# Kernel tuning notes

Hardware: AMD Instinct MI355X
Metric: run time of the kernel (lower is better)

## Reference

```python
import jax, jax.numpy as jnp
import numpy as np

B, S, N, F, H, O = 4, 16, 1024, 64, 128, 64
L_LAYERS, N_HEADS, CHUNK = 3, 4, 128
EPS = 1e-5


def setup_inputs() -> dict:
    key = jax.random.key(0)
    ks = jax.random.split(key, 16)
    adj = (jax.random.uniform(ks[0], (B, S, N, N)) < 0.05).astype(jnp.float32)
    adj = adj * (1.0 - jnp.eye(N, dtype=jnp.float32))
    x = jax.random.normal(ks[1], (B, S, F), dtype=jnp.float32)
    mask = jnp.ones((B, S), dtype=jnp.float32)
    sd = lambda fan_in: 1.0 / np.sqrt(fan_in)
    inp = {
        "x": x, "adj": adj, "mask": mask,
        "feature_importance": jnp.ones((F,), jnp.float32),
        "W_in": jax.random.normal(ks[2], (F, H)) * sd(F),
        "b_in": jnp.zeros((H,), jnp.float32),
        "ln_g": jnp.ones((H,), jnp.float32),
        "ln_b": jnp.zeros((H,), jnp.float32),
        "gcn_W": jax.random.normal(ks[3], (L_LAYERS, H, H)) * sd(H),
        "gcn_b": jnp.zeros((L_LAYERS, H), jnp.float32),
        "bn_g": jnp.ones((L_LAYERS, H), jnp.float32),
        "bn_b": jnp.zeros((L_LAYERS, H), jnp.float32),
        "Wqkv": jax.random.normal(ks[4], (3 * H, H)) * sd(H),
        "bqkv": jnp.zeros((3 * H,), jnp.float32),
        "Wo": jax.random.normal(ks[5], (H, H)) * sd(H),
        "bo": jnp.zeros((H,), jnp.float32),
        "W_out": jax.random.normal(ks[6], (H, O)) * sd(H),
        "b_out": jnp.zeros((O,), jnp.float32),
    }
    return inp


def _chunked_mha(h, Wqkv, bqkv, Wo, bo):
    # h: [B,S,N,H]; attention within chunks of CHUNK nodes (torch MHA, eval mode)
    b, s, n, hdim = h.shape
    c, dh = n // CHUNK, hdim // N_HEADS
    xr = h.reshape(b, s, c, CHUNK, hdim)
    qkv = xr @ Wqkv.T + bqkv                      # [B,S,C,L,3H]
    q, k, v = jnp.split(qkv, 3, axis=-1)
    split = lambda t: t.reshape(b, s, c, CHUNK, N_HEADS, dh).swapaxes(-3, -2)  # [B,S,C,nh,L,dh]
    q, k, v = split(q) * (dh ** -0.5), split(k), split(v)
    attn = jax.nn.softmax(jnp.einsum('bscnld,bscnmd->bscnlm', q, k), axis=-1)
    o = jnp.einsum('bscnlm,bscnmd->bscnld', attn, v)
    o = o.swapaxes(-3, -2).reshape(b, s, c, CHUNK, hdim) @ Wo.T + bo
    return o.reshape(b, s, n, hdim)


def reference(x, adj, mask, feature_importance, W_in, b_in, ln_g, ln_b,
              gcn_W, gcn_b, bn_g, bn_b, Wqkv, bqkv, Wo, bo, W_out, b_out):
    b, s, f = x.shape
    n = adj.shape[-1]
    # feature scaling + input projection + layer norm (same vector for all nodes)
    xv = (x * feature_importance) @ W_in + b_in            # [B,S,H]
    mu = xv.mean(-1, keepdims=True)
    var = ((xv - mu) ** 2).mean(-1, keepdims=True)
    hv = (xv - mu) / jnp.sqrt(var + EPS) * ln_g + ln_b
    h = jnp.broadcast_to(hv[:, :, None, :], (b, s, n, hv.shape[-1]))  # [B,S,N,H]
    h_init = h
    # GCN normalization: D^{-1/2} (A + I) D^{-1/2}
    A_hat = adj + jnp.eye(n, dtype=adj.dtype)
    dinv = jax.lax.rsqrt(A_hat.sum(-1))                     # [B,S,N]
    A_norm = dinv[..., :, None] * A_hat * dinv[..., None, :]
    bn_scale = 1.0 / np.sqrt(1.0 + EPS)  # eval BN, running mean 0 / var 1
    for l in range(L_LAYERS):
        hw = h @ gcn_W[l]
        hc = jnp.einsum('bsnm,bsmh->bsnh', A_norm, hw) + gcn_b[l]
        hc = hc * bn_scale * bn_g[l] + bn_b[l]
        hc = _chunked_mha(hc, Wqkv, bqkv, Wo, bo)
        hc = jax.nn.relu(hc)  # dropout = identity in eval
        h = h + hc            # use_skip (num_layers > 1)
    h = h + h_init
    node_embeddings = h @ W_out + b_out                    # [B,S,N,O]
    graph_embeddings = node_embeddings.mean(axis=2)        # [B,S,O]
    graph_embeddings = graph_embeddings * mask[:, :, None]
    node_embeddings = node_embeddings * mask[:, :, None, None]
    return node_embeddings, graph_embeddings
```

## Files before the change

kernel.cpp:

```cpp
#include <hip/hip_runtime.h>

typedef __bf16 bf16_t;
typedef bf16_t bf16x8 __attribute__((ext_vector_type(8)));
typedef float f32x4 __attribute__((ext_vector_type(4)));

#define DEV static __device__ __forceinline__

constexpr float kBnScale = 0.999995000037499375f;

DEV unsigned short f2bf(float f) {
  unsigned u = __builtin_bit_cast(unsigned, f);
  u += 0x7fffu + ((u >> 16) & 1u);
  return (unsigned short)(u >> 16);
}
DEV float bf2f(unsigned short s) {
  return __builtin_bit_cast(float, ((unsigned)s) << 16);
}
DEV f32x4 mfma16(bf16x8 a, bf16x8 b, f32x4 c) {
  return __builtin_amdgcn_mfma_f32_16x16x32_bf16(a, b, c, 0, 0, 0);
}
DEV unsigned swz(unsigned byteoff, unsigned row) { return byteoff ^ ((row & 7u) << 4); }

__global__ __launch_bounds__(256) void k_pre(
    const float* __restrict__ adj, unsigned short* __restrict__ cols,
    int* __restrict__ cnt, float* __restrict__ dinv,
    const float* __restrict__ x, const float* __restrict__ fi,
    const float* __restrict__ Win, const float* __restrict__ bin,
    const float* __restrict__ lng, const float* __restrict__ lnb,
    const float* __restrict__ gW, const float* __restrict__ bng,
    float* __restrict__ hv, float* __restrict__ hw0s,
    const float* __restrict__ Wqkv, const float* __restrict__ Wo,
    const float* __restrict__ Wout,
    unsigned short* __restrict__ WqkvB, unsigned short* __restrict__ WoB,
    unsigned short* __restrict__ gWB, unsigned short* __restrict__ WoutB) {
  const int bid = blockIdx.x;
  if (bid < 16384) {
    const int w = threadIdx.x >> 6, lane = threadIdx.x & 63;
    const long row = (long)bid * 4 + w;
    const float* ap = adj + row * 1024;
    unsigned short* cp = cols + row * 128;
    int c = 0;
#pragma unroll
    for (int it = 0; it < 4; ++it) {
      const float4 v4 = *(const float4*)(ap + it * 256 + lane * 4);
      const float vv[4] = {v4.x, v4.y, v4.z, v4.w};
#pragma unroll
      for (int j = 0; j < 4; ++j) {
        const unsigned long long m = __ballot(vv[j] != 0.0f);
        const int pos = c + __popcll(m & ((1ull << lane) - 1ull));
        if (vv[j] != 0.0f && pos < 128) cp[pos] = (unsigned short)(it * 256 + lane * 4 + j);
        c += __popcll(m);
      }
    }
    if (lane == 0) {
      cnt[row] = c;
      dinv[row] = 1.0f / sqrtf((float)(c + 1));
    }
  } else if (bid < 16448) {
    __shared__ float sred[2], sred2[2], shv[128];
    const int bs = bid - 16384, t = threadIdx.x;
    float accv = 0.f, d = 0.f;
    if (t < 128) {
      accv = bin[t];
      for (int f = 0; f < 64; ++f) accv += x[bs * 64 + f] * fi[f] * Win[f * 128 + t];
      float ssum = accv;
      for (int m = 1; m < 64; m <<= 1) ssum += __shfl_xor(ssum, m);
      if ((t & 63) == 0) sred[t >> 6] = ssum;
    }
    __syncthreads();
    const float mu = (sred[0] + sred[1]) * (1.0f / 128.0f);
    if (t < 128) {
      d = accv - mu;
      float vs = d * d;
      for (int m = 1; m < 64; m <<= 1) vs += __shfl_xor(vs, m);
      if ((t & 63) == 0) sred2[t >> 6] = vs;
    }
    __syncthreads();
    const float var = (sred2[0] + sred2[1]) * (1.0f / 128.0f);
    if (t < 128) {
      const float h = d / sqrtf(var + 1e-5f) * lng[t] + lnb[t];
      hv[bs * 128 + t] = h;
      shv[t] = h;
    }
    __syncthreads();
    if (t < 128) {
      float a2 = 0.f;
      for (int k = 0; k < 128; ++k) a2 += shv[k] * gW[k * 128 + t];
      hw0s[bs * 128 + t] = a2 * kBnScale * bng[t];
    }
  } else {
    const int i = (bid - 16448) * 256 + threadIdx.x;
    if (i < 49152) {
      WqkvB[i] = f2bf(Wqkv[i]);
    } else if (i < 65536) {
      const int j = i - 49152;
      WoB[j] = f2bf(Wo[j]);
    } else if (i < 114688) {
      const int j = i - 65536, l = j >> 14, r = j & 16383, n = r >> 7, k = r & 127;
      gWB[j] = f2bf(gW[(l << 14) + k * 128 + n]);
    } else {
      const int j = i - 114688, n = j >> 7, k = j & 127;
      WoutB[j] = f2bf(Wout[k * 64 + n]);
    }
  }
}

__global__ __launch_bounds__(256) void k_scal(const unsigned short* __restrict__ cols,
                                              const int* __restrict__ cnt, const float* __restrict__ dinv,
                                              float* __restrict__ S) {
  const int w = threadIdx.x >> 6, lane = threadIdx.x & 63;
  const long row = (long)blockIdx.x * 4 + w;
  const int cn = cnt[row] < 128 ? cnt[row] : 128;
  const long bsbase = row & ~1023L;
  const int c0 = cols[row * 128 + lane];
  const int c1 = cols[row * 128 + 64 + lane];
  float s = 0.f;
  if (lane < cn) s += dinv[bsbase + c0];
  if (lane + 64 < cn) s += dinv[bsbase + c1];
  for (int m = 1; m < 64; m <<= 1) s += __shfl_xor(s, m);
  if (lane == 0) {
    const float d = dinv[row];
    S[row] = d * (d + s);
  }
}

template <bool L0>
__global__ __launch_bounds__(256) void k_qkv(const unsigned short* __restrict__ hc,
                                             const unsigned short* __restrict__ WqkvB,
                                             const float* __restrict__ bqkv,
                                             const float* __restrict__ S, const float* __restrict__ hw0s,
                                             const float* __restrict__ gb0, const float* __restrict__ bng0,
                                             const float* __restrict__ bnb0,
                                             unsigned short* __restrict__ qkvb) {
  __shared__ __align__(16) unsigned short Ab[128 * 128];
  __shared__ __align__(16) unsigned short Bb[128 * 128];
  const int t = threadIdx.x;
  const long blockRow = (long)blockIdx.x * 128;
  const int pan = blockIdx.y;
  const int bs = (int)(blockRow >> 10);

  if constexpr (L0) {
#pragma unroll
    for (int i = 0; i < 16; ++i) {
      const int f = (t + i * 256) * 4;
      const unsigned row = f >> 7, k = f & 127;
      const float Sr = S[blockRow + row];
      const float4 hw = *(const float4*)(hw0s + bs * 128 + k);
      const float4 gv = *(const float4*)(gb0 + k);
      const float4 bg = *(const float4*)(bng0 + k);
      const float4 bb = *(const float4*)(bnb0 + k);
      float4 v;
      v.x = Sr * hw.x + (gv.x * kBnScale * bg.x + bb.x);
      v.y = Sr * hw.y + (gv.y * kBnScale * bg.y + bb.y);
      v.z = Sr * hw.z + (gv.z * kBnScale * bg.z + bb.z);
      v.w = Sr * hw.w + (gv.w * kBnScale * bg.w + bb.w);
      uint2 u;
      u.x = f2bf(v.x) | ((unsigned)f2bf(v.y) << 16);
      u.y = f2bf(v.z) | ((unsigned)f2bf(v.w) << 16);
      *(uint2*)(Ab + (swz(row * 256u + k * 2u, row) >> 1)) = u;
    }
  } else {
#pragma unroll
    for (int i = 0; i < 8; ++i) {
      const int f = (t + i * 256) * 8;
      const unsigned row = f >> 7, k = f & 127;
      *(uint4*)(Ab + (swz(row * 256u + k * 2u, row) >> 1)) = *(const uint4*)(hc + blockRow * 128 + f);
    }
  }
#pragma unroll
  for (int i = 0; i < 8; ++i) {
    const int f = (t + i * 256) * 8;
    const unsigned n = f >> 7, k = f & 127;
    *(uint4*)(Bb + (swz(n * 256u + k * 2u, n) >> 1)) = *(const uint4*)(WqkvB + pan * 16384 + f);
  }
  __syncthreads();

  const int lane = t & 63, w = t >> 6, wr = w >> 1, wc = w & 1;
  const f32x4 vzero = {0.f, 0.f, 0.f, 0.f};
  f32x4 acc[4][4];
#pragma unroll
  for (int a = 0; a < 4; ++a)
#pragma unroll
    for (int b = 0; b < 4; ++b) acc[a][b] = vzero;
#pragma unroll
  for (int kk = 0; kk < 4; ++kk) {
    const unsigned kb = kk * 64u + (unsigned)((lane >> 4) << 4);
    bf16x8 af[4], bfr[4];
#pragma unroll
    for (int mt = 0; mt < 4; ++mt) {
      const unsigned row = wr * 64 + mt * 16 + (lane & 15);
      af[mt] = *(const bf16x8*)(Ab + (swz(row * 256u + kb, row) >> 1));
    }
#pragma unroll
    for (int nt = 0; nt < 4; ++nt) {
      const unsigned col = wc * 64 + nt * 16 + (lane & 15);
      bfr[nt] = *(const bf16x8*)(Bb + (swz(col * 256u + kb, col) >> 1));
    }
#pragma unroll
    for (int mt = 0; mt < 4; ++mt)
#pragma unroll
      for (int nt = 0; nt < 4; ++nt) acc[mt][nt] = mfma16(af[mt], bfr[nt], acc[mt][nt]);
  }
#pragma unroll
  for (int mt = 0; mt < 4; ++mt)
#pragma unroll
    for (int nt = 0; nt < 4; ++nt)
#pragma unroll
      for (int r = 0; r < 4; ++r) {
        const long gRow = blockRow + wr * 64 + mt * 16 + ((lane >> 4) << 2) + r;
        const int gCol = wc * 64 + nt * 16 + (lane & 15);
        qkvb[gRow * 384 + pan * 128 + gCol] = f2bf(acc[mt][nt][r] + bqkv[pan * 128 + gCol]);
      }
}

__global__ __launch_bounds__(256) void k_spmm(const unsigned* __restrict__ hwp,
                                              const unsigned short* __restrict__ cols,
                                              const int* __restrict__ cnt, const float* __restrict__ dinv,
                                              const float* __restrict__ gb, const float* __restrict__ bng,
                                              const float* __restrict__ bnb, unsigned* __restrict__ hc) {
  int b = blockIdx.x;
  b = (b & 7) * 2048 + (b >> 3);
  const int w = threadIdx.x >> 6, lane = threadIdx.x & 63;
  const long row = (long)b * 4 + w;
  __shared__ unsigned short scol[4][128];
  scol[w][lane] = cols[row * 128 + lane];
  scol[w][lane + 64] = cols[row * 128 + 64 + lane];
  const int cn = cnt[row] < 128 ? cnt[row] : 128;
  const long bsbase = row & ~1023L;
  const unsigned us = hwp[row * 64 + lane];
  float a0 = bf2f((unsigned short)us), a1 = bf2f((unsigned short)(us >> 16));
  int i = 0;
  for (; i + 4 <= cn; i += 4) {
    const uint2 jj = *(const uint2*)(&scol[w][i]);
    const int j0 = jj.x & 0xffff, j1 = jj.x >> 16, j2 = jj.y & 0xffff, j3 = jj.y >> 16;
    const unsigned u0 = hwp[(bsbase + j0) * 64 + lane];
    const unsigned u1 = hwp[(bsbase + j1) * 64 + lane];
    const unsigned u2 = hwp[(bsbase + j2) * 64 + lane];
    const unsigned u3 = hwp[(bsbase + j3) * 64 + lane];
    a0 += bf2f((unsigned short)u0) + bf2f((unsigned short)u1) + bf2f((unsigned short)u2) + bf2f((unsigned short)u3);
    a1 += bf2f((unsigned short)(u0 >> 16)) + bf2f((unsigned short)(u1 >> 16)) +
          bf2f((unsigned short)(u2 >> 16)) + bf2f((unsigned short)(u3 >> 16));
  }
  for (; i < cn; ++i) {
    const unsigned uu = hwp[(bsbase + scol[w][i]) * 64 + lane];
    a0 += bf2f((unsigned short)uu);
    a1 += bf2f((unsigned short)(uu >> 16));
  }
  const float di = dinv[row];
  const int c0 = lane * 2, c1 = c0 + 1;
  const float o0 = (di * a0 + gb[c0]) * (kBnScale * bng[c0]) + bnb[c0];
  const float o1 = (di * a1 + gb[c1]) * (kBnScale * bng[c1]) + bnb[c1];
  hc[row * 64 + lane] = (unsigned)f2bf(o0) | ((unsigned)f2bf(o1) << 16);
}

template <int MODE>
__global__ __launch_bounds__(256, 2) void k_af(
    const unsigned short* __restrict__ qkv,
    const unsigned short* __restrict__ WoB, const unsigned short* __restrict__ B2,
    const float* __restrict__ bo, const float* __restrict__ hv,
    const float* __restrict__ dinv, const float* __restrict__ bout,
    const float* __restrict__ mask,
    float* __restrict__ hbuf, unsigned short* __restrict__ hwp,
    float* __restrict__ ne, float* __restrict__ gpart) {
  __shared__ __align__(16) unsigned short sm[32768];
  unsigned short* Ab = sm;
  unsigned short* Bb = sm + 16384;
  const int t = threadIdx.x, lane = t & 63, hd = t >> 6;
  const int g = lane >> 4, l15 = lane & 15;
  const long cb = (long)blockIdx.x * 128;
  const int bs = (int)(cb >> 10);
  const f32x4 vzero = {0.f, 0.f, 0.f, 0.f};

  {
    const int m = t >> 1, half = t & 1;
    const unsigned short* vrow = qkv + (cb + m) * 384 + 256 + half * 64;
#pragma unroll
    for (int c8 = 0; c8 < 8; ++c8) {
      const uint4 u = *(const uint4*)(vrow + c8 * 8);
      const int col0 = half * 64 + c8 * 8;
      unsigned short* vb = Ab + (col0 >> 5) * 4096;
      const int dh0 = col0 & 31;
      const unsigned short e[8] = {(unsigned short)u.x, (unsigned short)(u.x >> 16),
                                   (unsigned short)u.y, (unsigned short)(u.y >> 16),
                                   (unsigned short)u.z, (unsigned short)(u.z >> 16),
                                   (unsigned short)u.w, (unsigned short)(u.w >> 16)};
#pragma unroll
      for (int j = 0; j < 8; ++j) {
        const unsigned dh = dh0 + j;
        vb[swz(dh * 256u + (unsigned)m * 2u, dh) >> 1] = e[j];
      }
    }
  }
  bf16x8 kf[8];
#pragma unroll
  for (int nt = 0; nt < 8; ++nt)
    kf[nt] = *(const bf16x8*)(qkv + (cb + nt * 16 + l15) * 384 + 128 + hd * 32 + (g << 3));
  __syncthreads();

  const unsigned short* vbb = Ab + hd * 4096;
  unsigned short* pb = Bb + hd * 4096;
  const float SC = 0.17677669529663687f * 1.4426950408889634f;
  unsigned pk[4][2][2][2];

#pragma unroll 1
  for (int p = 0; p < 4; ++p) {
    bf16x8 qf[2];
#pragma unroll
    for (int mt = 0; mt < 2; ++mt)
      qf[mt] = *(const bf16x8*)(qkv + (cb + p * 32 + mt * 16 + l15) * 384 + hd * 32 + (g << 3));
    f32x4 s[2][8];
#pragma unroll
    for (int mt = 0; mt < 2; ++mt)
#pragma unroll
      for (int nt = 0; nt < 8; ++nt) s[mt][nt] = vzero;
#pragma unroll
    for (int nt = 0; nt < 8; ++nt)
#pragma unroll
      for (int mt = 0; mt < 2; ++mt) s[mt][nt] = mfma16(qf[mt], kf[nt], s[mt][nt]);

    float rinv[2][4];
#pragma unroll
    for (int mt = 0; mt < 2; ++mt) {
#pragma unroll
      for (int r = 0; r < 4; ++r) {
        float mx = s[mt][0][r];
#pragma unroll
        for (int nt = 1; nt < 8; ++nt) mx = fmaxf(mx, s[mt][nt][r]);
#pragma unroll
        for (int msk = 1; msk < 16; msk <<= 1) mx = fmaxf(mx, __shfl_xor(mx, msk));
        const unsigned qp = mt * 16 + g * 4 + r;
        float sum = 0.f;
#pragma unroll
        for (int nt = 0; nt < 8; ++nt) {
          const float e = exp2f((s[mt][nt][r] - mx) * SC);
          sum += e;
          pb[swz(qp * 256u + (nt * 16 + l15) * 2u, qp) >> 1] = f2bf(e);
        }
#pragma unroll
        for (int msk = 1; msk < 16; msk <<= 1) sum += __shfl_xor(sum, msk);
        rinv[mt][r] = 1.0f / sum;
      }
    }

    f32x4 o[2][2];
#pragma unroll
    for (int mt = 0; mt < 2; ++mt)
#pragma unroll
      for (int nt = 0; nt < 2; ++nt) o[mt][nt] = vzero;
#pragma unroll
    for (int kk = 0; kk < 4; ++kk) {
      const unsigned kb = kk * 64u + (unsigned)(g << 4);
      bf16x8 pa[2], vf[2];
#pragma unroll
      for (int mt = 0; mt < 2; ++mt) {
        const unsigned rq = mt * 16 + l15;
        pa[mt] = *(const bf16x8*)(pb + (swz(rq * 256u + kb, rq) >> 1));
      }
#pragma unroll
      for (int nt = 0; nt < 2; ++nt) {
        const unsigned dh = nt * 16 + l15;
        vf[nt] = *(const bf16x8*)(vbb + (swz(dh * 256u + kb, dh) >> 1));
      }
#pragma unroll
      for (int mt = 0; mt < 2; ++mt)
#pragma unroll
        for (int nt = 0; nt < 2; ++nt) o[mt][nt] = mfma16(pa[mt], vf[nt], o[mt][nt]);
    }
#pragma unroll
    for (int mt = 0; mt < 2; ++mt)
#pragma unroll
      for (int nt = 0; nt < 2; ++nt) {
        pk[p][mt][nt][0] = (unsigned)f2bf(o[mt][nt][0] * rinv[mt][0]) |
                           ((unsigned)f2bf(o[mt][nt][1] * rinv[mt][1]) << 16);
        pk[p][mt][nt][1] = (unsigned)f2bf(o[mt][nt][2] * rinv[mt][2]) |
                           ((unsigned)f2bf(o[mt][nt][3] * rinv[mt][3]) << 16);
      }
  }
  __syncthreads();

#pragma unroll
  for (int p = 0; p < 4; ++p)
#pragma unroll
    for (int mt = 0; mt < 2; ++mt)
#pragma unroll
      for (int nt = 0; nt < 2; ++nt)
#pragma unroll
        for (int rr = 0; rr < 2; ++rr) {
          const unsigned u = pk[p][mt][nt][rr];
          const unsigned row0 = p * 32 + mt * 16 + g * 4 + rr * 2;
          const unsigned col = hd * 32 + nt * 16 + l15;
          Ab[swz(row0 * 256u + col * 2u, row0) >> 1] = (unsigned short)u;
          Ab[swz((row0 + 1) * 256u + col * 2u, row0 + 1) >> 1] = (unsigned short)(u >> 16);
        }
#pragma unroll
  for (int i = 0; i < 8; ++i) {
    const int f = (t + i * 256) * 8;
    const unsigned n = f >> 7, k = f & 127;
    *(uint4*)(Bb + (swz(n * 256u + k * 2u, n) >> 1)) = *(const uint4*)(WoB + f);
  }
  __syncthreads();

  const int wr = hd >> 1, wc = hd & 1;
  f32x4 acc[4][4];
#pragma unroll
  for (int a = 0; a < 4; ++a)
#pragma unroll
    for (int b = 0; b < 4; ++b) acc[a][b] = vzero;
#pragma unroll
  for (int kk = 0; kk < 4; ++kk) {
    const unsigned kb = kk * 64u + (unsigned)(g << 4);
    bf16x8 af[4], bfr[4];
#pragma unroll
    for (int mt = 0; mt < 4; ++mt) {
      const unsigned row = wr * 64 + mt * 16 + l15;
      af[mt] = *(const bf16x8*)(Ab + (swz(row * 256u + kb, row) >> 1));
    }
#pragma unroll
    for (int nt = 0; nt < 4; ++nt) {
      const unsigned col = wc * 64 + nt * 16 + l15;
      bfr[nt] = *(const bf16x8*)(Bb + (swz(col * 256u + kb, col) >> 1));
    }
#pragma unroll
    for (int mt = 0; mt < 4; ++mt)
#pragma unroll
      for (int nt = 0; nt < 4; ++nt) acc[mt][nt] = mfma16(af[mt], bfr[nt], acc[mt][nt]);
  }
  __syncthreads();

  {
    const float b0 = bo[wc * 64 + l15], b1 = bo[wc * 64 + 16 + l15];
    const float b2c = bo[wc * 64 + 32 + l15], b3c = bo[wc * 64 + 48 + l15];
    const float bb[4] = {b0, b1, b2c, b3c};
    float hb[4];
#pragma unroll
    for (int nt = 0; nt < 4; ++nt) hb[nt] = hv[bs * 128 + wc * 64 + nt * 16 + l15];
#pragma unroll
    for (int mt = 0; mt < 4; ++mt)
#pragma unroll
      for (int nt = 0; nt < 4; ++nt)
#pragma unroll
        for (int r = 0; r < 4; ++r) {
          const unsigned row = wr * 64 + mt * 16 + g * 4 + r;
          const long gRow = cb + row;
          const unsigned col = wc * 64 + nt * 16 + l15;
          float v = acc[mt][nt][r] + bb[nt];
          v = v > 0.f ? v : 0.f;
          if constexpr (MODE == 0) {
            v += hb[nt];
          } else {
            v += hbuf[gRow * 128 + col];
            if constexpr (MODE == 2) v += hb[nt];
          }
          if constexpr (MODE < 2) hbuf[gRow * 128 + col] = v;
          Ab[swz(row * 256u + col * 2u, row) >> 1] = f2bf(v);
        }
  }
  if constexpr (MODE < 2) {
#pragma unroll
    for (int i = 0; i < 8; ++i) {
      const int f = (t + i * 256) * 8;
      const unsigned n = f >> 7, k = f & 127;
      *(uint4*)(Bb + (swz(n * 256u + k * 2u, n) >> 1)) = *(const uint4*)(B2 + f);
    }
  } else {
#pragma unroll
    for (int i = 0; i < 4; ++i) {
      const int f = (t + i * 256) * 8;
      const unsigned n = f >> 7, k = f & 127;
      *(uint4*)(Bb + (swz(n * 256u + k * 2u, n) >> 1)) = *(const uint4*)(B2 + f);
    }
  }
  __syncthreads();

  if constexpr (MODE < 2) {
#pragma unroll
    for (int a = 0; a < 4; ++a)
#pragma unroll
      for (int b = 0; b < 4; ++b) acc[a][b] = vzero;
#pragma unroll
    for (int kk = 0; kk < 4; ++kk) {
      const unsigned kb = kk * 64u + (unsigned)(g << 4);
      bf16x8 af[4], bfr[4];
#pragma unroll
      for (int mt = 0; mt < 4; ++mt) {
        const unsigned row = wr * 64 + mt * 16 + l15;
        af[mt] = *(const bf16x8*)(Ab + (swz(row * 256u + kb, row) >> 1));
      }
#pragma unroll
      for (int nt = 0; nt < 4; ++nt) {
        const unsigned col = wc * 64 + nt * 16 + l15;
        bfr[nt] = *(const bf16x8*)(Bb + (swz(col * 256u + kb, col) >> 1));
      }
#pragma unroll
      for (int mt = 0; mt < 4; ++mt)
#pragma unroll
        for (int nt = 0; nt < 4; ++nt) acc[mt][nt] = mfma16(af[mt], bfr[nt], acc[mt][nt]);
    }
#pragma unroll
    for (int mt = 0; mt < 4; ++mt)
#pragma unroll
      for (int nt = 0; nt < 4; ++nt)
#pragma unroll
        for (int r = 0; r < 4; ++r) {
          const long gRow = cb + wr * 64 + mt * 16 + g * 4 + r;
          const unsigned col = wc * 64 + nt * 16 + l15;
          hwp[gRow * 128 + col] = f2bf(acc[mt][nt][r] * dinv[gRow]);
        }
  } else {
    f32x4 acc2[4][2];
#pragma unroll
    for (int a = 0; a < 4; ++a)
#pragma unroll
      for (int b = 0; b < 2; ++b) acc2[a][b] = vzero;
#pragma unroll
    for (int kk = 0; kk < 4; ++kk) {
      const unsigned kb = kk * 64u + (unsigned)(g << 4);
      bf16x8 af[4], bfr[2];
#pragma unroll
      for (int mt = 0; mt < 4; ++mt) {
        const unsigned row = wr * 64 + mt * 16 + l15;
        af[mt] = *(const bf16x8*)(Ab + (swz(row * 256u + kb, row) >> 1));
      }
#pragma unroll
      for (int nt = 0; nt < 2; ++nt) {
        const unsigned col = wc * 32 + nt * 16 + l15;
        bfr[nt] = *(const bf16x8*)(Bb + (swz(col * 256u + kb, col) >> 1));
      }
#pragma unroll
      for (int mt = 0; mt < 4; ++mt)
#pragma unroll
        for (int nt = 0; nt < 2; ++nt) acc2[mt][nt] = mfma16(af[mt], bfr[nt], acc2[mt][nt]);
    }
    const float mk = mask[bs];
#pragma unroll
    for (int nt = 0; nt < 2; ++nt) {
      const unsigned col = wc * 32 + nt * 16 + l15;
      const float b2 = bout[col];
      float csum = 0.f;
#pragma unroll
      for (int mt = 0; mt < 4; ++mt)
#pragma unroll
        for (int r = 0; r < 4; ++r) {
          const long gRow = cb + wr * 64 + mt * 16 + g * 4 + r;
          const float v = (acc2[mt][nt][r] + b2) * mk;
          ne[gRow * 64 + col] = v;
          csum += v;
        }
      csum += __shfl_xor(csum, 16);
      csum += __shfl_xor(csum, 32);
      if (g == 0) gpart[((long)blockIdx.x * 2 + wr) * 64 + col] = csum;
    }
  }
}

__global__ void k_gfin(const float* __restrict__ gpart, float* __restrict__ ge) {
  const int tid = blockIdx.x * 256 + threadIdx.x;
  if (tid >= 4096) return;
  const int bs = tid >> 6, col = tid & 63;
  float s = 0.f;
#pragma unroll
  for (int q = 0; q < 16; ++q) s += gpart[(bs * 16 + q) * 64 + col];
  ge[tid] = s * (1.0f / 1024.0f);
}

extern "C" void kernel_launch(void* const* d_in, const int* in_sizes, int n_in,
                              void* d_out, int out_size, void* d_ws, size_t ws_size,
                              hipStream_t stream) {
  const float* x = (const float*)d_in[0];
  const float* adj = (const float*)d_in[1];
  const float* mask = (const float*)d_in[2];
  const float* fi = (const float*)d_in[3];
  const float* Win = (const float*)d_in[4];
  const float* bin = (const float*)d_in[5];
  const float* lng = (const float*)d_in[6];
  const float* lnb = (const float*)d_in[7];
  const float* gW = (const float*)d_in[8];
  const float* gB = (const float*)d_in[9];
  const float* bng = (const float*)d_in[10];
  const float* bnb = (const float*)d_in[11];
  const float* Wqkv = (const float*)d_in[12];
  const float* bqkv = (const float*)d_in[13];
  const float* Wo = (const float*)d_in[14];
  const float* bo = (const float*)d_in[15];
  const float* Wout = (const float*)d_in[16];
  const float* bout = (const float*)d_in[17];

  char* ws = (char*)d_ws;
  float* dinv = (float*)ws;                    ws += 65536 * 4;
  int* cnt = (int*)ws;                         ws += 65536 * 4;
  float* S = (float*)ws;                       ws += 65536 * 4;
  float* hv = (float*)ws;                      ws += 64 * 128 * 4;
  float* hw0s = (float*)ws;                    ws += 64 * 128 * 4;
  float* gpart = (float*)ws;                   ws += 1024 * 64 * 4;
  unsigned short* WqkvB = (unsigned short*)ws; ws += 49152 * 2;
  unsigned short* WoB = (unsigned short*)ws;   ws += 16384 * 2;
  unsigned short* gWB = (unsigned short*)ws;   ws += 49152 * 2;
  unsigned short* WoutB = (unsigned short*)ws; ws += 8192 * 2;
  unsigned short* cols = (unsigned short*)ws;  ws += (size_t)65536 * 128 * 2;
  float* hbuf = (float*)ws;                    ws += (size_t)65536 * 128 * 4;
  unsigned short* hwp = (unsigned short*)ws;   ws += (size_t)65536 * 128 * 2;
  unsigned short* hc = (unsigned short*)ws;    ws += (size_t)65536 * 128 * 2;
  unsigned short* qkvb = (unsigned short*)ws;  ws += (size_t)65536 * 384 * 2;

  float* ne = (float*)d_out;
  float* ge = ne + (size_t)4194304;

  k_pre<<<16928, 256, 0, stream>>>(adj, cols, cnt, dinv, x, fi, Win, bin, lng, lnb,
                                   gW, bng, hv, hw0s, Wqkv, Wo, Wout,
                                   WqkvB, WoB, gWB, WoutB);
  k_scal<<<16384, 256, 0, stream>>>(cols, cnt, dinv, S);

  k_qkv<true><<<dim3(512, 3), 256, 0, stream>>>(nullptr, WqkvB, bqkv, S, hw0s, gB, bng, bnb, qkvb);
  k_af<0><<<512, 256, 0, stream>>>(qkvb, WoB, gWB + 16384, bo, hv, dinv, nullptr, nullptr,
                                   hbuf, hwp, nullptr, nullptr);
  k_spmm<<<16384, 256, 0, stream>>>((const unsigned*)hwp, cols, cnt, dinv,
                                    gB + 128, bng + 128, bnb + 128, (unsigned*)hc);
  k_qkv<false><<<dim3(512, 3), 256, 0, stream>>>(hc, WqkvB, bqkv, nullptr, nullptr, nullptr, nullptr, nullptr, qkvb);
  k_af<1><<<512, 256, 0, stream>>>(qkvb, WoB, gWB + 32768, bo, hv, dinv, nullptr, nullptr,
                                   hbuf, hwp, nullptr, nullptr);
  k_spmm<<<16384, 256, 0, stream>>>((const unsigned*)hwp, cols, cnt, dinv,
                                    gB + 256, bng + 256, bnb + 256, (unsigned*)hc);
  k_qkv<false><<<dim3(512, 3), 256, 0, stream>>>(hc, WqkvB, bqkv, nullptr, nullptr, nullptr, nullptr, nullptr, qkvb);
  k_af<2><<<512, 256, 0, stream>>>(qkvb, WoB, WoutB, bo, hv, dinv, bout, mask,
                                   hbuf, nullptr, ne, gpart);

  k_gfin<<<16, 256, 0, stream>>>(gpart, ge);
}
```

Measured before the change: 362.6 us.

## Vectorize SpMM gathers, remap blocks across XCDs, fuse layer-0 input into scaling kernel

The SpMM gather now has each 16-lane group fetch a whole 256-byte row as uint4 loads, with four neighbours handled in parallel and the partial sums combined by cross-lane shuffles. Before, each lane did a 4-byte load per neighbour. The scaling kernel now writes the layer-0 bf16 GCN output directly, so the QKV GEMM no longer needs a special first-layer path or the S buffer. Block indices in several kernels are permuted so that consecutive work lands on the same XCD, which should improve L2 locality. The costs are extra shuffle reductions and one more global write and read of the layer-0 activations.

```diff
diff --git a/kernel.cpp b/kernel.cpp
--- a/kernel.cpp
+++ b/kernel.cpp
@@ -35,8 +35,9 @@
     unsigned short* __restrict__ gWB, unsigned short* __restrict__ WoutB) {
   const int bid = blockIdx.x;
   if (bid < 16384) {
+    const int c4 = (bid & 7) * 2048 + (bid >> 3);
     const int w = threadIdx.x >> 6, lane = threadIdx.x & 63;
-    const long row = (long)bid * 4 + w;
+    const long row = (long)c4 * 4 + w;
     const float* ap = adj + row * 1024;
     unsigned short* cp = cols + row * 128;
     int c = 0;
@@ -105,11 +106,16 @@
   }
 }
 
-__global__ __launch_bounds__(256) void k_scal(const unsigned short* __restrict__ cols,
-                                              const int* __restrict__ cnt, const float* __restrict__ dinv,
-                                              float* __restrict__ S) {
+__global__ __launch_bounds__(256) void k_scal2(const unsigned short* __restrict__ cols,
+                                               const int* __restrict__ cnt, const float* __restrict__ dinv,
+                                               const float* __restrict__ hw0s,
+                                               const float* __restrict__ gb0, const float* __restrict__ bng0,
+                                               const float* __restrict__ bnb0,
+                                               unsigned* __restrict__ hc0) {
+  int b = blockIdx.x;
+  b = (b & 7) * 2048 + (b >> 3);
   const int w = threadIdx.x >> 6, lane = threadIdx.x & 63;
-  const long row = (long)blockIdx.x * 4 + w;
+  const long row = (long)b * 4 + w;
   const int cn = cnt[row] < 128 ? cnt[row] : 128;
   const long bsbase = row & ~1023L;
   const int c0 = cols[row * 128 + lane];
@@ -118,59 +124,35 @@
   if (lane < cn) s += dinv[bsbase + c0];
   if (lane + 64 < cn) s += dinv[bsbase + c1];
   for (int m = 1; m < 64; m <<= 1) s += __shfl_xor(s, m);
-  if (lane == 0) {
-    const float d = dinv[row];
-    S[row] = d * (d + s);
-  }
-}
-
-template <bool L0>
+  const float d = dinv[row];
+  const float S = d * (d + s);
+  const int bs = (int)(row >> 10);
+  const float2 hw = ((const float2*)hw0s)[bs * 64 + lane];
+  const float2 g2 = ((const float2*)gb0)[lane];
+  const float2 bg = ((const float2*)bng0)[lane];
+  const float2 bb = ((const float2*)bnb0)[lane];
+  const float v0 = S * hw.x + (g2.x * kBnScale * bg.x + bb.x);
+  const float v1 = S * hw.y + (g2.y * kBnScale * bg.y + bb.y);
+  hc0[row * 64 + lane] = (unsigned)f2bf(v0) | ((unsigned)f2bf(v1) << 16);
+}
+
 __global__ __launch_bounds__(256) void k_qkv(const unsigned short* __restrict__ hc,
                                              const unsigned short* __restrict__ WqkvB,
                                              const float* __restrict__ bqkv,
-                                             const float* __restrict__ S, const float* __restrict__ hw0s,
-                                             const float* __restrict__ gb0, const float* __restrict__ bng0,
-                                             const float* __restrict__ bnb0,
                                              unsigned short* __restrict__ qkvb) {
   __shared__ __align__(16) unsigned short Ab[128 * 128];
   __shared__ __align__(16) unsigned short Bb[128 * 128];
   const int t = threadIdx.x;
-  const long blockRow = (long)blockIdx.x * 128;
+  const int cx = (blockIdx.x & 7) * 64 + (blockIdx.x >> 3);
+  const long blockRow = (long)cx * 128;
   const int pan = blockIdx.y;
-  const int bs = (int)(blockRow >> 10);
-
-  if constexpr (L0) {
-#pragma unroll
-    for (int i = 0; i < 16; ++i) {
-      const int f = (t + i * 256) * 4;
-      const unsigned row = f >> 7, k = f & 127;
-      const float Sr = S[blockRow + row];
-      const float4 hw = *(const float4*)(hw0s + bs * 128 + k);
-      const float4 gv = *(const float4*)(gb0 + k);
-      const float4 bg = *(const float4*)(bng0 + k);
-      const float4 bb = *(const float4*)(bnb0 + k);
-      float4 v;
-      v.x = Sr * hw.x + (gv.x * kBnScale * bg.x + bb.x);
-      v.y = Sr * hw.y + (gv.y * kBnScale * bg.y + bb.y);
-      v.z = Sr * hw.z + (gv.z * kBnScale * bg.z + bb.z);
-      v.w = Sr * hw.w + (gv.w * kBnScale * bg.w + bb.w);
-      uint2 u;
-      u.x = f2bf(v.x) | ((unsigned)f2bf(v.y) << 16);
-      u.y = f2bf(v.z) | ((unsigned)f2bf(v.w) << 16);
-      *(uint2*)(Ab + (swz(row * 256u + k * 2u, row) >> 1)) = u;
-    }
-  } else {
-#pragma unroll
-    for (int i = 0; i < 8; ++i) {
-      const int f = (t + i * 256) * 8;
-      const unsigned row = f >> 7, k = f & 127;
-      *(uint4*)(Ab + (swz(row * 256u + k * 2u, row) >> 1)) = *(const uint4*)(hc + blockRow * 128 + f);
-    }
-  }
+
 #pragma unroll
   for (int i = 0; i < 8; ++i) {
     const int f = (t + i * 256) * 8;
-    const unsigned n = f >> 7, k = f & 127;
+    const unsigned row = f >> 7, k = f & 127;
+    *(uint4*)(Ab + (swz(row * 256u + k * 2u, row) >> 1)) = *(const uint4*)(hc + blockRow * 128 + f);
+    const unsigned n = row;
     *(uint4*)(Bb + (swz(n * 256u + k * 2u, n) >> 1)) = *(const uint4*)(WqkvB + pan * 16384 + f);
   }
   __syncthreads();
@@ -213,44 +195,81 @@
       }
 }
 
-__global__ __launch_bounds__(256) void k_spmm(const unsigned* __restrict__ hwp,
+__global__ __launch_bounds__(256) void k_spmm(const uint4* __restrict__ hwp16,
                                               const unsigned short* __restrict__ cols,
                                               const int* __restrict__ cnt, const float* __restrict__ dinv,
                                               const float* __restrict__ gb, const float* __restrict__ bng,
-                                              const float* __restrict__ bnb, unsigned* __restrict__ hc) {
+                                              const float* __restrict__ bnb, uint4* __restrict__ hc16) {
   int b = blockIdx.x;
   b = (b & 7) * 2048 + (b >> 3);
   const int w = threadIdx.x >> 6, lane = threadIdx.x & 63;
+  const int g = lane >> 4, l15 = lane & 15;
   const long row = (long)b * 4 + w;
   __shared__ unsigned short scol[4][128];
   scol[w][lane] = cols[row * 128 + lane];
   scol[w][lane + 64] = cols[row * 128 + 64 + lane];
   const int cn = cnt[row] < 128 ? cnt[row] : 128;
   const long bsbase = row & ~1023L;
-  const unsigned us = hwp[row * 64 + lane];
-  float a0 = bf2f((unsigned short)us), a1 = bf2f((unsigned short)(us >> 16));
-  int i = 0;
-  for (; i + 4 <= cn; i += 4) {
-    const uint2 jj = *(const uint2*)(&scol[w][i]);
-    const int j0 = jj.x & 0xffff, j1 = jj.x >> 16, j2 = jj.y & 0xffff, j3 = jj.y >> 16;
-    const unsigned u0 = hwp[(bsbase + j0) * 64 + lane];
-    const unsigned u1 = hwp[(bsbase + j1) * 64 + lane];
-    const unsigned u2 = hwp[(bsbase + j2) * 64 + lane];
-    const unsigned u3 = hwp[(bsbase + j3) * 64 + lane];
-    a0 += bf2f((unsigned short)u0) + bf2f((unsigned short)u1) + bf2f((unsigned short)u2) + bf2f((unsigned short)u3);
-    a1 += bf2f((unsigned short)(u0 >> 16)) + bf2f((unsigned short)(u1 >> 16)) +
-          bf2f((unsigned short)(u2 >> 16)) + bf2f((unsigned short)(u3 >> 16));
-  }
-  for (; i < cn; ++i) {
-    const unsigned uu = hwp[(bsbase + scol[w][i]) * 64 + lane];
-    a0 += bf2f((unsigned short)uu);
-    a1 += bf2f((unsigned short)(uu >> 16));
-  }
-  const float di = dinv[row];
-  const int c0 = lane * 2, c1 = c0 + 1;
-  const float o0 = (di * a0 + gb[c0]) * (kBnScale * bng[c0]) + bnb[c0];
-  const float o1 = (di * a1 + gb[c1]) * (kBnScale * bng[c1]) + bnb[c1];
-  hc[row * 64 + lane] = (unsigned)f2bf(o0) | ((unsigned)f2bf(o1) << 16);
+  float acc[8];
+#pragma unroll
+  for (int e = 0; e < 8; ++e) acc[e] = 0.f;
+  if (g == 0) {
+    const uint4 u = hwp16[row * 16 + l15];
+    const unsigned uu[4] = {u.x, u.y, u.z, u.w};
+#pragma unroll
+    for (int e2 = 0; e2 < 4; ++e2) {
+      acc[e2 * 2] += bf2f((unsigned short)uu[e2]);
+      acc[e2 * 2 + 1] += bf2f((unsigned short)(uu[e2] >> 16));
+    }
+  }
+  const int cn4 = cn & ~3;
+#pragma unroll 2
+  for (int i = 0; i < cn4; i += 4) {
+    const int j = scol[w][i + g];
+    const uint4 u = hwp16[(bsbase + j) * 16 + l15];
+    const unsigned uu[4] = {u.x, u.y, u.z, u.w};
+#pragma unroll
+    for (int e2 = 0; e2 < 4; ++e2) {
+      acc[e2 * 2] += bf2f((unsigned short)uu[e2]);
+      acc[e2 * 2 + 1] += bf2f((unsigned short)(uu[e2] >> 16));
+    }
+  }
+  if (cn4 + g < cn) {
+    const int j = scol[w][cn4 + g];
+    const uint4 u = hwp16[(bsbase + j) * 16 + l15];
+    const unsigned uu[4] = {u.x, u.y, u.z, u.w};
+#pragma unroll
+    for (int e2 = 0; e2 < 4; ++e2) {
+      acc[e2 * 2] += bf2f((unsigned short)uu[e2]);
+      acc[e2 * 2 + 1] += bf2f((unsigned short)(uu[e2] >> 16));
+    }
+  }
+#pragma unroll
+  for (int e = 0; e < 8; ++e) {
+    acc[e] += __shfl_xor(acc[e], 16);
+    acc[e] += __shfl_xor(acc[e], 32);
+  }
+  if (g == 0) {
+    const float di = dinv[row];
+    const float4 gv0 = ((const float4*)gb)[l15 * 2], gv1 = ((const float4*)gb)[l15 * 2 + 1];
+    const float4 bg0 = ((const float4*)bng)[l15 * 2], bg1 = ((const float4*)bng)[l15 * 2 + 1];
+    const float4 bb0 = ((const float4*)bnb)[l15 * 2], bb1 = ((const float4*)bnb)[l15 * 2 + 1];
+    float o[8];
+    o[0] = (di * acc[0] + gv0.x) * (kBnScale * bg0.x) + bb0.x;
+    o[1] = (di * acc[1] + gv0.y) * (kBnScale * bg0.y) + bb0.y;
+    o[2] = (di * acc[2] + gv0.z) * (kBnScale * bg0.z) + bb0.z;
+    o[3] = (di * acc[3] + gv0.w) * (kBnScale * bg0.w) + bb0.w;
+    o[4] = (di * acc[4] + gv1.x) * (kBnScale * bg1.x) + bb1.x;
+    o[5] = (di * acc[5] + gv1.y) * (kBnScale * bg1.y) + bb1.y;
+    o[6] = (di * acc[6] + gv1.z) * (kBnScale * bg1.z) + bb1.z;
+    o[7] = (di * acc[7] + gv1.w) * (kBnScale * bg1.w) + bb1.w;
+    uint4 r;
+    r.x = (unsigned)f2bf(o[0]) | ((unsigned)f2bf(o[1]) << 16);
+    r.y = (unsigned)f2bf(o[2]) | ((unsigned)f2bf(o[3]) << 16);
+    r.z = (unsigned)f2bf(o[4]) | ((unsigned)f2bf(o[5]) << 16);
+    r.w = (unsigned)f2bf(o[6]) | ((unsigned)f2bf(o[7]) << 16);
+    hc16[row * 16 + l15] = r;
+  }
 }
 
 template <int MODE>
@@ -267,7 +286,8 @@
   unsigned short* Bb = sm + 16384;
   const int t = threadIdx.x, lane = t & 63, hd = t >> 6;
   const int g = lane >> 4, l15 = lane & 15;
-  const long cb = (long)blockIdx.x * 128;
+  const int c = (blockIdx.x & 7) * 64 + (blockIdx.x >> 3);
+  const long cb = (long)c * 128;
   const int bs = (int)(cb >> 10);
   const f32x4 vzero = {0.f, 0.f, 0.f, 0.f};
 
@@ -548,7 +568,7 @@
         }
       csum += __shfl_xor(csum, 16);
       csum += __shfl_xor(csum, 32);
-      if (g == 0) gpart[((long)blockIdx.x * 2 + wr) * 64 + col] = csum;
+      if (g == 0) gpart[((long)c * 2 + wr) * 64 + col] = csum;
     }
   }
 }
@@ -588,7 +608,6 @@
   char* ws = (char*)d_ws;
   float* dinv = (float*)ws;                    ws += 65536 * 4;
   int* cnt = (int*)ws;                         ws += 65536 * 4;
-  float* S = (float*)ws;                       ws += 65536 * 4;
   float* hv = (float*)ws;                      ws += 64 * 128 * 4;
   float* hw0s = (float*)ws;                    ws += 64 * 128 * 4;
   float* gpart = (float*)ws;                   ws += 1024 * 64 * 4;
@@ -608,19 +627,19 @@
   k_pre<<<16928, 256, 0, stream>>>(adj, cols, cnt, dinv, x, fi, Win, bin, lng, lnb,
                                    gW, bng, hv, hw0s, Wqkv, Wo, Wout,
                                    WqkvB, WoB, gWB, WoutB);
-  k_scal<<<16384, 256, 0, stream>>>(cols, cnt, dinv, S);
-
-  k_qkv<true><<<dim3(512, 3), 256, 0, stream>>>(nullptr, WqkvB, bqkv, S, hw0s, gB, bng, bnb, qkvb);
+  k_scal2<<<16384, 256, 0, stream>>>(cols, cnt, dinv, hw0s, gB, bng, bnb, (unsigned*)hc);
+
+  k_qkv<<<dim3(512, 3), 256, 0, stream>>>(hc, WqkvB, bqkv, qkvb);
   k_af<0><<<512, 256, 0, stream>>>(qkvb, WoB, gWB + 16384, bo, hv, dinv, nullptr, nullptr,
                                    hbuf, hwp, nullptr, nullptr);
-  k_spmm<<<16384, 256, 0, stream>>>((const unsigned*)hwp, cols, cnt, dinv,
-                                    gB + 128, bng + 128, bnb + 128, (unsigned*)hc);
-  k_qkv<false><<<dim3(512, 3), 256, 0, stream>>>(hc, WqkvB, bqkv, nullptr, nullptr, nullptr, nullptr, nullptr, qkvb);
+  k_spmm<<<16384, 256, 0, stream>>>((const uint4*)hwp, cols, cnt, dinv,
+                                    gB + 128, bng + 128, bnb + 128, (uint4*)hc);
+  k_qkv<<<dim3(512, 3), 256, 0, stream>>>(hc, WqkvB, bqkv, qkvb);
   k_af<1><<<512, 256, 0, stream>>>(qkvb, WoB, gWB + 32768, bo, hv, dinv, nullptr, nullptr,
                                    hbuf, hwp, nullptr, nullptr);
-  k_spmm<<<16384, 256, 0, stream>>>((const unsigned*)hwp, cols, cnt, dinv,
-                                    gB + 256, bng + 256, bnb + 256, (unsigned*)hc);
-  k_qkv<false><<<dim3(512, 3), 256, 0, stream>>>(hc, WqkvB, bqkv, nullptr, nullptr, nullptr, nullptr, nullptr, qkvb);
+  k_spmm<<<16384, 256, 0, stream>>>((const uint4*)hwp, cols, cnt, dinv,
+                                    gB + 256, bng + 256, bnb + 256, (uint4*)hc);
+  k_qkv<<<dim3(512, 3), 256, 0, stream>>>(hc, WqkvB, bqkv, qkvb);
   k_af<2><<<512, 256, 0, stream>>>(qkvb, WoB, WoutB, bo, hv, dinv, bout, mask,
                                    hbuf, nullptr, ne, gpart);
 
```

Measured after the change: 349.8 us. 3.5% less time.
